# Kernel optimization log

Measured on AMD Instinct MI355X. Metric: run time of the kernel, lower is better.

The kernel has to match this reference:

```python
import jax, jax.numpy as jnp
import numpy as np

N = 50000      # nodes
E = 800000     # edges (avg degree 16)
F_IN = 128     # input feature dim
HID = 64       # hidden_channels
HEADS = 4
OUT = 64       # out_channels


def _gatv2_layer(x, src, dst, Wl, Wr, att, bias, heads, ch, n):
    # lin_l (source) and lin_r (target) projections -> [N, H, C]
    xl = (x @ Wl).reshape(n, heads, ch)
    xr = (x @ Wr).reshape(n, heads, ch)
    # per-edge GATv2 attention logits: a^T LeakyReLU(xl_j + xr_i)
    e = jax.nn.leaky_relu(xl[src] + xr[dst], negative_slope=0.2)  # [E, H, C]
    score = jnp.einsum('ehc,hc->eh', e, att)                      # [E, H]
    # segment softmax over incoming edges of each destination node
    m = jax.ops.segment_max(score, dst, num_segments=n)           # [N, H]
    m = jnp.where(jnp.isfinite(m), m, 0.0)
    p = jnp.exp(score - m[dst])
    denom = jax.ops.segment_sum(p, dst, num_segments=n)           # [N, H]
    alpha = p / (denom[dst] + 1e-16)                              # [E, H]
    # weighted scatter-aggregate of source messages xl_j
    out = jax.ops.segment_sum(alpha[..., None] * xl[src], dst, num_segments=n)
    return out.reshape(n, heads * ch) + bias


def setup_inputs() -> dict:
    key = jax.random.key(0)
    ks = jax.random.split(key, 16)

    def w(k, shape, fan_in):
        return (jax.random.normal(k, shape, dtype=jnp.float32) / np.sqrt(fan_in)).astype(jnp.float32)

    return {
        'x': jax.random.normal(ks[0], (N, F_IN), dtype=jnp.float32),
        'Wl1': w(ks[1], (F_IN, HEADS * HID), F_IN),
        'Wr1': w(ks[2], (F_IN, HEADS * HID), F_IN),
        'att1': w(ks[3], (HEADS, HID), HID),
        'b1': jnp.zeros((HEADS * HID,), jnp.float32),
        'Wl2': w(ks[4], (HEADS * HID, HEADS * HID), HEADS * HID),
        'Wr2': w(ks[5], (HEADS * HID, HEADS * HID), HEADS * HID),
        'att2': w(ks[6], (HEADS, HID), HID),
        'b2': jnp.zeros((HEADS * HID,), jnp.float32),
        'Wl3': w(ks[7], (HEADS * HID, OUT), HEADS * HID),
        'Wr3': w(ks[8], (HEADS * HID, OUT), HEADS * HID),
        'att3': w(ks[9], (1, OUT), OUT),
        'b3': jnp.zeros((OUT,), jnp.float32),
        'Wlin': w(ks[10], (OUT, HID), OUT),
        'blin': jnp.zeros((HID,), jnp.float32),
        'edge_index': jax.random.randint(ks[11], (2, E), 0, N, dtype=jnp.int64
                                         if jax.config.read('jax_enable_x64') else jnp.int32),
    }


def reference(x, Wl1, Wr1, att1, b1, Wl2, Wr2, att2, b2, Wl3, Wr3, att3, b3, Wlin, blin, edge_index):
    src, dst = edge_index[0], edge_index[1]
    h = jax.nn.elu(_gatv2_layer(x, src, dst, Wl1, Wr1, att1, b1, HEADS, HID, N))
    h = jax.nn.elu(_gatv2_layer(h, src, dst, Wl2, Wr2, att2, b2, HEADS, HID, N))
    h = _gatv2_layer(h, src, dst, Wl3, Wr3, att3, b3, 1, OUT, N)
    # F.dropout(p=0.5, training=False) -> identity in eval mode
    return h @ Wlin + blin
```

## Files before the change

kernel.cpp:

```cpp
#include <hip/hip_runtime.h>
#include <hip/hip_fp16.h>

#define NN 50000
#define EE 800000

typedef float f32x4 __attribute__((ext_vector_type(4)));
typedef _Float16 f16x8 __attribute__((ext_vector_type(8)));
typedef _Float16 f16x4 __attribute__((ext_vector_type(4)));
typedef _Float16 f16x2 __attribute__((ext_vector_type(2)));

__global__ void hist_kernel(const int* __restrict__ dst, int* __restrict__ counts, int E) {
    int idx = blockIdx.x * blockDim.x + threadIdx.x;
    int stride = gridDim.x * blockDim.x;
    for (int e = idx; e < E; e += stride)
        atomicAdd(&counts[dst[e]], 1);
}

__global__ void scan_kernel(const int* __restrict__ counts, int* __restrict__ row_off, int n) {
    __shared__ int sums[1024];
    int t = threadIdx.x;
    int chunk = (n + 1023) >> 10;
    int lo = t * chunk;
    int hi = min(lo + chunk, n);
    int s = 0;
    for (int i = lo; i < hi; ++i) s += counts[i];
    sums[t] = s;
    __syncthreads();
    for (int off = 1; off < 1024; off <<= 1) {
        int v = (t >= off) ? sums[t - off] : 0;
        __syncthreads();
        sums[t] += v;
        __syncthreads();
    }
    int run = (t == 0) ? 0 : sums[t - 1];
    for (int i = lo; i < hi; ++i) { row_off[i] = run; run += counts[i]; }
    if (t == 1023) row_off[n] = sums[1023];
}

__global__ void scatter_kernel(const int* __restrict__ src, const int* __restrict__ dst,
                               const int* __restrict__ row_off, int* __restrict__ cursor,
                               int* __restrict__ esrc, int E) {
    int idx = blockIdx.x * blockDim.x + threadIdx.x;
    int stride = gridDim.x * blockDim.x;
    for (int e = idx; e < E; e += stride) {
        int d = dst[e];
        int pos = row_off[d] + atomicAdd(&cursor[d], 1);
        esrc[pos] = src[e];
    }
}

__device__ __forceinline__ void wfrag_store(__half* o, int K, int col, int k, float v) {
    int KS = K >> 5;
    int cgni = col >> 4, l15 = col & 15;
    int ks = k >> 5, qq = (k >> 3) & 3, ee = k & 7;
    size_t flat = ((size_t)(cgni * KS + ks) * 64 + qq * 16 + l15) * 8 + ee;
    o[flat] = __float2half_rn(v);
}

__global__ void prep_all(const float* __restrict__ Wl1, const float* __restrict__ Wr1,
                         const float* __restrict__ Wl2, const float* __restrict__ Wr2,
                         const float* __restrict__ Wl3, const float* __restrict__ Wr3,
                         const float* __restrict__ Wlin,
                         __half* __restrict__ w1, __half* __restrict__ w2,
                         __half* __restrict__ w3, __half* __restrict__ w4,
                         const float* __restrict__ x, __half* __restrict__ xf, int n4x) {
    int idx = blockIdx.x * blockDim.x + threadIdx.x;
    if (idx < 233472) {
        const float* W; __half* o; int K, Nc, roff, li;
        if (idx < 65536) {
            K = 128; Nc = 256; o = w1;
            if (idx < 32768) { W = Wl1; li = idx; roff = 0; }
            else             { W = Wr1; li = idx - 32768; roff = 256; }
        } else if (idx < 196608) {
            K = 256; Nc = 256; o = w2;
            if (idx < 131072) { W = Wl2; li = idx - 65536; roff = 0; }
            else              { W = Wr2; li = idx - 131072; roff = 256; }
        } else if (idx < 229376) {
            K = 256; Nc = 64; o = w3;
            if (idx < 212992) { W = Wl3; li = idx - 196608; roff = 0; }
            else              { W = Wr3; li = idx - 212992; roff = 64; }
        } else {
            K = 64; Nc = 64; o = w4; W = Wlin; li = idx - 229376; roff = 0;
        }
        int k = li / Nc, n = li - k * Nc;
        wfrag_store(o, K, roff + n, k, W[li]);
    } else {
        int xi = idx - 233472;
        if (xi < n4x) {
            float4 v = *(const float4*)(x + (size_t)xi * 4);
            f16x4 h = {(_Float16)v.x, (_Float16)v.y, (_Float16)v.z, (_Float16)v.w};
            *(f16x4*)((_Float16*)xf + (size_t)xi * 4) = h;
        }
    }
}

template <int KS, int COLG>
__global__ __launch_bounds__(COLG * 256) void gemm_ws(
        const __half* __restrict__ A, const __half* __restrict__ Bt,
        int M, int nTiles, int Nc, int splitCol,
        __half* __restrict__ outL, __half* __restrict__ outR,
        float* __restrict__ outF, const float* __restrict__ bias) {
    constexpr int K = KS * 32;
    int tid = threadIdx.x;
    int lane = tid & 63;
    int w = tid >> 6;
    int rs = w & 3;
    int cg = w >> 2;
    int l15 = lane & 15, q = lane >> 4;
    int colbase = blockIdx.y * (COLG * 64) + cg * 64;

    const _Float16* Ap = (const _Float16*)A;
    const f16x8* Bf = (const f16x8*)Bt;
    int cgni0 = (blockIdx.y * COLG + cg) * 4;

    f16x8 bfrag[KS][4];
#pragma unroll
    for (int ks = 0; ks < KS; ++ks)
#pragma unroll
        for (int ni = 0; ni < 4; ++ni)
            bfrag[ks][ni] = Bf[((size_t)(cgni0 + ni) * KS + ks) * 64 + lane];

    int tile = blockIdx.x;
    if (tile >= nTiles) return;

    f16x8 afrag[KS];
    {
        int row = tile * 64 + rs * 16 + l15;
        if (row >= M) row = M - 1;
        const _Float16* ap = Ap + (size_t)row * K + q * 8;
#pragma unroll
        for (int ks = 0; ks < KS; ++ks) afrag[ks] = *(const f16x8*)(ap + ks * 32);
    }

    while (true) {
        int next = tile + gridDim.x;
        bool has = (next < nTiles);
        f16x8 anext[KS];
        if (has) {
            int row = next * 64 + rs * 16 + l15;
            if (row >= M) row = M - 1;
            const _Float16* ap = Ap + (size_t)row * K + q * 8;
#pragma unroll
            for (int ks = 0; ks < KS; ++ks) anext[ks] = *(const f16x8*)(ap + ks * 32);
        }

        f32x4 acc[4] = {};
#pragma unroll
        for (int ks = 0; ks < KS; ++ks)
#pragma unroll
            for (int ni = 0; ni < 4; ++ni)
                acc[ni] = __builtin_amdgcn_mfma_f32_16x16x32_f16(afrag[ks], bfrag[ks][ni], acc[ni], 0, 0, 0);

#pragma unroll
        for (int ni = 0; ni < 4; ++ni) {
            int gc = colbase + ni * 16 + l15;
            if (outF) {
                float bv = bias ? bias[gc] : 0.f;
#pragma unroll
                for (int r = 0; r < 4; ++r) {
                    int gr = tile * 64 + rs * 16 + q * 4 + r;
                    if (gr < M) outF[(size_t)gr * Nc + gc] = acc[ni][r] + bv;
                }
            } else {
                __half* dp = outL; int cc = gc;
                if (gc >= splitCol) { dp = outR; cc = gc - splitCol; }
#pragma unroll
                for (int r = 0; r < 4; ++r) {
                    int gr = tile * 64 + rs * 16 + q * 4 + r;
                    if (gr < M) dp[(size_t)gr * splitCol + cc] = __float2half_rn(acc[ni][r]);
                }
            }
        }
        if (!has) break;
#pragma unroll
        for (int ks = 0; ks < KS; ++ks) afrag[ks] = anext[ks];
        tile = next;
    }
}

__global__ __launch_bounds__(256) void gat_gather_h4(
        const __half* __restrict__ xl, const __half* __restrict__ xr,
        const float* __restrict__ att, const float* __restrict__ bias,
        const int* __restrict__ row_off, const int* __restrict__ esrc,
        __half* __restrict__ out, int n) {
    const float LOG2E = 1.44269504f;
    int wave = threadIdx.x >> 6;
    int lane = threadIdx.x & 63;
    int node = blockIdx.x * 4 + wave;
    if (node >= n) return;
    int half = lane >> 5;
    unsigned j = lane & 31;

    const uint4* xl4 = (const uint4*)xl;
    uint4 xraw = ((const uint4*)xr)[((unsigned)node << 5) + j];
    f16x2 xrv[4] = {*(const f16x2*)&xraw.x, *(const f16x2*)&xraw.y,
                    *(const f16x2*)&xraw.z, *(const f16x2*)&xraw.w};
    float4 aA = *(const float4*)(att + j * 8);
    float4 aB = *(const float4*)(att + j * 8 + 4);
    f16x2 atv[4] = {{(_Float16)(aA.x * LOG2E), (_Float16)(aA.y * LOG2E)},
                    {(_Float16)(aA.z * LOG2E), (_Float16)(aA.w * LOG2E)},
                    {(_Float16)(aB.x * LOG2E), (_Float16)(aB.y * LOG2E)},
                    {(_Float16)(aB.z * LOG2E), (_Float16)(aB.w * LOG2E)}};
    const f16x2 k02 = {(_Float16)0.2f, (_Float16)0.2f};

    float acc0[8] = {}, acc1[8] = {};
    float l0 = 0.f, l1 = 0.f;

    int e0 = row_off[node], e1 = row_off[node + 1];
    int elast = e1 - 1;

#define H4_BODY(EBASE, ACC, LSUM)                                             \
    {                                                                         \
        int idx_ = EBASE + half;                                              \
        int s_ = esrc[min(idx_, elast)];                                      \
        uint4 raw_ = xl4[((unsigned)s_ << 5) + j];                            \
        f16x2 v0_ = *(const f16x2*)&raw_.x;                                   \
        f16x2 v1_ = *(const f16x2*)&raw_.y;                                   \
        f16x2 v2_ = *(const f16x2*)&raw_.z;                                   \
        f16x2 v3_ = *(const f16x2*)&raw_.w;                                   \
        f16x2 s0_ = v0_ + xrv[0], s1_ = v1_ + xrv[1];                         \
        f16x2 s2_ = v2_ + xrv[2], s3_ = v3_ + xrv[3];                         \
        f16x2 r0_ = __builtin_elementwise_max(s0_, s0_ * k02);                \
        f16x2 r1_ = __builtin_elementwise_max(s1_, s1_ * k02);                \
        f16x2 r2_ = __builtin_elementwise_max(s2_, s2_ * k02);                \
        f16x2 r3_ = __builtin_elementwise_max(s3_, s3_ * k02);                \
        float t_ = __builtin_amdgcn_fdot2(r0_, atv[0], 0.f, false);           \
        t_ = __builtin_amdgcn_fdot2(r1_, atv[1], t_, false);                  \
        t_ = __builtin_amdgcn_fdot2(r2_, atv[2], t_, false);                  \
        t_ = __builtin_amdgcn_fdot2(r3_, atv[3], t_, false);                  \
        t_ += __shfl_xor(t_, 1);                                              \
        t_ += __shfl_xor(t_, 2);                                              \
        t_ += __shfl_xor(t_, 4);                                              \
        float p_ = exp2f(t_);                                                 \
        p_ = (idx_ < e1) ? p_ : 0.f;                                          \
        LSUM += p_;                                                           \
        ACC[0] = fmaf((float)v0_.x, p_, ACC[0]);                              \
        ACC[1] = fmaf((float)v0_.y, p_, ACC[1]);                              \
        ACC[2] = fmaf((float)v1_.x, p_, ACC[2]);                              \
        ACC[3] = fmaf((float)v1_.y, p_, ACC[3]);                              \
        ACC[4] = fmaf((float)v2_.x, p_, ACC[4]);                              \
        ACC[5] = fmaf((float)v2_.y, p_, ACC[5]);                              \
        ACC[6] = fmaf((float)v3_.x, p_, ACC[6]);                              \
        ACC[7] = fmaf((float)v3_.y, p_, ACC[7]);                              \
    }

    for (int e = e0; e < e1; e += 4) {
        H4_BODY(e, acc0, l0)
        if (e + 2 < e1) H4_BODY(e + 2, acc1, l1)
    }
#undef H4_BODY

    float acc[8];
#pragma unroll
    for (int k = 0; k < 8; ++k) acc[k] = acc0[k] + acc1[k];
    float L = l0 + l1;
#pragma unroll
    for (int k = 0; k < 8; ++k) acc[k] += __shfl_xor(acc[k], 32);
    L += __shfl_xor(L, 32);

    float inv = 1.f / (L + 1e-16f);
    float4 bvA = *(const float4*)(bias + j * 8);
    float4 bvB = *(const float4*)(bias + j * 8 + 4);
    float bb[8] = {bvA.x, bvA.y, bvA.z, bvA.w, bvB.x, bvB.y, bvB.z, bvB.w};
    f16x8 ov;
#pragma unroll
    for (int k = 0; k < 8; ++k) {
        float v = acc[k] * inv + bb[k];
        v = v > 0.f ? v : __expf(v) - 1.f;
        ov[k] = (_Float16)v;
    }
    if (half == 0)
        ((f16x8*)((_Float16*)out + ((size_t)node << 8)))[j] = ov;
}

__global__ __launch_bounds__(256) void gat_gather_h1(
        const __half* __restrict__ xl, const __half* __restrict__ xr,
        const float* __restrict__ att, const float* __restrict__ bias,
        const int* __restrict__ row_off, const int* __restrict__ esrc,
        __half* __restrict__ out, int n) {
    const float LOG2E = 1.44269504f;
    int wave = threadIdx.x >> 6;
    int lane = threadIdx.x & 63;
    int node = blockIdx.x * 4 + wave;
    if (node >= n) return;
    int q4 = lane >> 4;
    unsigned j = lane & 15;

    const uint2* xl2 = (const uint2*)xl;
    uint2 xraw = ((const uint2*)xr)[((unsigned)node << 4) + j];
    f16x2 xrv[2] = {*(const f16x2*)&xraw.x, *(const f16x2*)&xraw.y};
    float4 av = *(const float4*)(att + j * 4);
    f16x2 atv[2] = {{(_Float16)(av.x * LOG2E), (_Float16)(av.y * LOG2E)},
                    {(_Float16)(av.z * LOG2E), (_Float16)(av.w * LOG2E)}};
    const f16x2 k02 = {(_Float16)0.2f, (_Float16)0.2f};

    float acc0[4] = {}, acc1[4] = {};
    float l0 = 0.f, l1 = 0.f;

    int e0 = row_off[node], e1 = row_off[node + 1];
    int elast = e1 - 1;

#define H1_BODY(EBASE, ACC, LSUM)                                             \
    {                                                                         \
        int idx_ = EBASE + q4;                                                \
        int s_ = esrc[min(idx_, elast)];                                      \
        uint2 raw_ = xl2[((unsigned)s_ << 4) + j];                            \
        f16x2 v0_ = *(const f16x2*)&raw_.x;                                   \
        f16x2 v1_ = *(const f16x2*)&raw_.y;                                   \
        f16x2 s0_ = v0_ + xrv[0], s1_ = v1_ + xrv[1];                         \
        f16x2 r0_ = __builtin_elementwise_max(s0_, s0_ * k02);                \
        f16x2 r1_ = __builtin_elementwise_max(s1_, s1_ * k02);                \
        float t_ = __builtin_amdgcn_fdot2(r0_, atv[0], 0.f, false);           \
        t_ = __builtin_amdgcn_fdot2(r1_, atv[1], t_, false);                  \
        t_ += __shfl_xor(t_, 1);                                              \
        t_ += __shfl_xor(t_, 2);                                              \
        t_ += __shfl_xor(t_, 4);                                              \
        t_ += __shfl_xor(t_, 8);                                              \
        float p_ = exp2f(t_);                                                 \
        p_ = (idx_ < e1) ? p_ : 0.f;                                          \
        LSUM += p_;                                                           \
        ACC[0] = fmaf((float)v0_.x, p_, ACC[0]);                              \
        ACC[1] = fmaf((float)v0_.y, p_, ACC[1]);                              \
        ACC[2] = fmaf((float)v1_.x, p_, ACC[2]);                              \
        ACC[3] = fmaf((float)v1_.y, p_, ACC[3]);                              \
    }

    for (int e = e0; e < e1; e += 8) {
        H1_BODY(e, acc0, l0)
        if (e + 4 < e1) H1_BODY(e + 4, acc1, l1)
    }
#undef H1_BODY

    float acc[4];
#pragma unroll
    for (int k = 0; k < 4; ++k) acc[k] = acc0[k] + acc1[k];
    float L = l0 + l1;
#pragma unroll
    for (int k = 0; k < 4; ++k) {
        acc[k] += __shfl_xor(acc[k], 16);
        acc[k] += __shfl_xor(acc[k], 32);
    }
    L += __shfl_xor(L, 16);
    L += __shfl_xor(L, 32);

    float inv = 1.f / (L + 1e-16f);
    float4 bv = *(const float4*)(bias + j * 4);
    f16x4 ov = {(_Float16)(acc[0] * inv + bv.x),
                (_Float16)(acc[1] * inv + bv.y),
                (_Float16)(acc[2] * inv + bv.z),
                (_Float16)(acc[3] * inv + bv.w)};
    if (q4 == 0)
        ((f16x4*)((_Float16*)out + ((size_t)node << 6)))[j] = ov;
}

extern "C" void kernel_launch(void* const* d_in, const int* in_sizes, int n_in,
                              void* d_out, int out_size, void* d_ws, size_t ws_size,
                              hipStream_t stream) {
    const float* x    = (const float*)d_in[0];
    const float* Wl1  = (const float*)d_in[1];
    const float* Wr1  = (const float*)d_in[2];
    const float* att1 = (const float*)d_in[3];
    const float* b1   = (const float*)d_in[4];
    const float* Wl2  = (const float*)d_in[5];
    const float* Wr2  = (const float*)d_in[6];
    const float* att2 = (const float*)d_in[7];
    const float* b2   = (const float*)d_in[8];
    const float* Wl3  = (const float*)d_in[9];
    const float* Wr3  = (const float*)d_in[10];
    const float* att3 = (const float*)d_in[11];
    const float* b3   = (const float*)d_in[12];
    const float* Wlin = (const float*)d_in[13];
    const float* blin = (const float*)d_in[14];
    const int*   ei   = (const int*)d_in[15];
    const int* src = ei;
    const int* dst = ei + EE;

    const int N = NN, E = EE;

    __half* xf = (__half*)d_ws;
    __half* xl = xf + (size_t)N * 128;
    __half* xr = xl + (size_t)N * 256;
    __half* H  = xr + (size_t)N * 256;
    __half* G  = H + (size_t)N * 256;
    __half* w1 = G + (size_t)N * 64;
    __half* w2 = w1 + 65536;
    __half* w3 = w2 + 131072;
    __half* w4 = w3 + 32768;
    int* row_off = (int*)(w4 + 4096);
    int* tmp     = row_off + (N + 1);
    int* esrc    = tmp + 2 * N;

    hipMemsetAsync(tmp, 0, (size_t)2 * N * sizeof(int), stream);
    hist_kernel<<<1024, 256, 0, stream>>>(dst, tmp, E);
    scan_kernel<<<1, 1024, 0, stream>>>(tmp, row_off, N);
    scatter_kernel<<<1024, 256, 0, stream>>>(src, dst, row_off, tmp + N, esrc, E);

    int n4x = N * 128 / 4;
    prep_all<<<(233472 + n4x + 255) / 256, 256, 0, stream>>>(
        Wl1, Wr1, Wl2, Wr2, Wl3, Wr3, Wlin, w1, w2, w3, w4, x, xf, n4x);

    int nTiles = (N + 63) / 64;
    int gatherBlocks = (N + 3) / 4;

    gemm_ws<4, 2><<<dim3(128, 4), 512, 0, stream>>>(
        xf, w1, N, nTiles, 512, 256, xl, xr, nullptr, nullptr);
    gat_gather_h4<<<gatherBlocks, 256, 0, stream>>>(xl, xr, att1, b1, row_off, esrc, H, N);

    gemm_ws<8, 2><<<dim3(128, 4), 512, 0, stream>>>(
        H, w2, N, nTiles, 512, 256, xl, xr, nullptr, nullptr);
    gat_gather_h4<<<gatherBlocks, 256, 0, stream>>>(xl, xr, att2, b2, row_off, esrc, H, N);

    gemm_ws<8, 2><<<dim3(256, 1), 512, 0, stream>>>(
        H, w3, N, nTiles, 128, 64, xl, xr, nullptr, nullptr);
    gat_gather_h1<<<gatherBlocks, 256, 0, stream>>>(xl, xr, att3, b3, row_off, esrc, G, N);

    gemm_ws<2, 1><<<dim3(512, 1), 256, 0, stream>>>(
        G, w4, N, nTiles, 64, 64, nullptr, nullptr, (float*)d_out, blin);
}
```

Measured before the change: 555.2 us.

## Replace single-block CSR prefix scan with three-phase multi-block scan

The exclusive prefix sum over per-node edge counts used to run in one 1024-thread block, where each thread serially walked a chunk of about 49 counts, twice. It is now split into three kernels: per-block reductions, a single-block scan of the 196 block sums, and per-block scans that add each block's offset. This spreads the scan across many CUs at the cost of two extra launches and a small bsum buffer placed after esrc in the workspace.

```diff
diff --git a/kernel.cpp b/kernel.cpp
--- a/kernel.cpp
+++ b/kernel.cpp
@@ -16,25 +16,53 @@
         atomicAdd(&counts[dst[e]], 1);
 }
 
-__global__ void scan_kernel(const int* __restrict__ counts, int* __restrict__ row_off, int n) {
-    __shared__ int sums[1024];
+__global__ void scan_phaseA(const int* __restrict__ counts, int* __restrict__ bsum, int n) {
+    __shared__ int buf[256];
+    int b = blockIdx.x, t = threadIdx.x;
+    int i = b * 256 + t;
+    buf[t] = (i < n) ? counts[i] : 0;
+    __syncthreads();
+#pragma unroll
+    for (int off = 128; off; off >>= 1) {
+        if (t < off) buf[t] += buf[t + off];
+        __syncthreads();
+    }
+    if (t == 0) bsum[b] = buf[0];
+}
+
+__global__ void scan_phaseB(int* __restrict__ bsum, int* __restrict__ row_off_n, int nb) {
+    __shared__ int buf[256];
     int t = threadIdx.x;
-    int chunk = (n + 1023) >> 10;
-    int lo = t * chunk;
-    int hi = min(lo + chunk, n);
-    int s = 0;
-    for (int i = lo; i < hi; ++i) s += counts[i];
-    sums[t] = s;
+    int v = (t < nb) ? bsum[t] : 0;
+    buf[t] = v;
     __syncthreads();
-    for (int off = 1; off < 1024; off <<= 1) {
-        int v = (t >= off) ? sums[t - off] : 0;
+#pragma unroll
+    for (int off = 1; off < 256; off <<= 1) {
+        int x = (t >= off) ? buf[t - off] : 0;
         __syncthreads();
-        sums[t] += v;
+        buf[t] += x;
         __syncthreads();
     }
-    int run = (t == 0) ? 0 : sums[t - 1];
-    for (int i = lo; i < hi; ++i) { row_off[i] = run; run += counts[i]; }
-    if (t == 1023) row_off[n] = sums[1023];
+    if (t < nb) bsum[t] = buf[t] - v;
+    if (t == 255) *row_off_n = buf[255];
+}
+
+__global__ void scan_phaseC(const int* __restrict__ counts, const int* __restrict__ bsum,
+                            int* __restrict__ row_off, int n) {
+    __shared__ int buf[256];
+    int b = blockIdx.x, t = threadIdx.x;
+    int i = b * 256 + t;
+    int v = (i < n) ? counts[i] : 0;
+    buf[t] = v;
+    __syncthreads();
+#pragma unroll
+    for (int off = 1; off < 256; off <<= 1) {
+        int x = (t >= off) ? buf[t - off] : 0;
+        __syncthreads();
+        buf[t] += x;
+        __syncthreads();
+    }
+    if (i < n) row_off[i] = bsum[b] + buf[t] - v;
 }
 
 __global__ void scatter_kernel(const int* __restrict__ src, const int* __restrict__ dst,
@@ -376,6 +404,7 @@
     const int* dst = ei + EE;
 
     const int N = NN, E = EE;
+    const int NB = (N + 255) / 256;
 
     __half* xf = (__half*)d_ws;
     __half* xl = xf + (size_t)N * 128;
@@ -389,10 +418,13 @@
     int* row_off = (int*)(w4 + 4096);
     int* tmp     = row_off + (N + 1);
     int* esrc    = tmp + 2 * N;
+    int* bsum    = esrc + E;
 
     hipMemsetAsync(tmp, 0, (size_t)2 * N * sizeof(int), stream);
     hist_kernel<<<1024, 256, 0, stream>>>(dst, tmp, E);
-    scan_kernel<<<1, 1024, 0, stream>>>(tmp, row_off, N);
+    scan_phaseA<<<NB, 256, 0, stream>>>(tmp, bsum, N);
+    scan_phaseB<<<1, 256, 0, stream>>>(bsum, row_off + N, NB);
+    scan_phaseC<<<NB, 256, 0, stream>>>(tmp, bsum, row_off, N);
     scatter_kernel<<<1024, 256, 0, stream>>>(src, dst, row_off, tmp + N, esrc, E);
 
     int n4x = N * 128 / 4;
```

After: 494.7 us. 1.12x faster.
